# Optimization experiments

Hardware: AMD Instinct MI355X
Metric: run time of the kernel (lower is better)

## Reference

```python
import jax, jax.numpy as jnp
import numpy as np
import math


def setup_inputs() -> dict:
    key = jax.random.key(0)
    k1, k2 = jax.random.split(key)
    N, FEATS, K = 100000, 256, 2000
    node_embs = jax.random.normal(k1, (N, FEATS), dtype=jnp.float32)
    # mask of zeros = all nodes valid (original uses -inf for invalid nodes)
    mask = jnp.zeros((N, 1), dtype=jnp.float32)
    # scorer param, uniform(-stdv, stdv) with stdv = 1/sqrt(feats), as in reset_param
    stdv = 1.0 / math.sqrt(FEATS)
    scorer = jax.random.uniform(k2, (FEATS, 1), minval=-stdv, maxval=stdv, dtype=jnp.float32)
    return {"node_embs": node_embs, "mask": mask, "scorer": scorer, "k": K}


def reference(node_embs, mask, scorer, k):
    # scores: [N,1] = (node_embs @ scorer) / sum(scorer) + mask
    scores = (node_embs @ scorer) / jnp.sum(scorer) + mask
    # top-k over flattened scores (column dim is 1, so indices == node indices)
    vals, topk_indices = jax.lax.top_k(scores.ravel(), k)
    # NOTE: original filters vals > -inf (drops masked-out picks); with a finite
    # (all-zeros) mask every selected entry passes, so shape stays static [k].
    out = jnp.take(node_embs, topk_indices, axis=0)  # [k, feats]
    return out.T  # [feats, k]
```

## Files before the change

kernel.cpp:

```cpp
#include <hip/hip_runtime.h>
#include <stdint.h>


#define NBINS 8192
#define BIN_SHIFT 19
#define CAP 4096
#define HPARTS 8

__device__ __forceinline__ uint32_t f2key(float f) {
  uint32_t b = __float_as_uint(f);
  return (b & 0x80000000u) ? ~b : (b | 0x80000000u);
}

__global__ __launch_bounds__(256) void k1_scores(
    const float* __restrict__ embs, const float* __restrict__ mask,
    const float* __restrict__ scorer,
    uint32_t* __restrict__ keys, uint32_t* __restrict__ hdr, int N) {
  __shared__ float tile[32 * 132];
  __shared__ float sw[256];
  __shared__ float Ssh;
  int t = threadIdx.x;
  int r0 = blockIdx.x * 32;
  if (blockIdx.x == 0 && t < 16) hdr[t] = 0u;
  sw[t] = scorer[t];
  __syncthreads();
  if (t < 64) {
    double s = 0.0;
    for (int j = t; j < 256; j += 64) s += (double)sw[j];
#pragma unroll
    for (int off = 32; off >= 1; off >>= 1) s += __shfl_xor(s, off, 64);
    if (t == 0) Ssh = (float)s;
  }
  __syncthreads();
  float S = Ssh;
  int r = t >> 3, c = t & 7;
  float acc = 0.f;
  const float4* e4 = (const float4*)embs;
#pragma unroll
  for (int ch = 0; ch < 2; ++ch) {
    if (ch) __syncthreads();
#pragma unroll
    for (int m = 0; m < 4; ++m) {
      int flat = m * 256 + t;
      int rr = flat >> 5;
      int cc4 = flat & 31;
      int row = r0 + rr;
      float4 v = make_float4(0.f, 0.f, 0.f, 0.f);
      if (row < N) v = e4[(size_t)row * 64 + ch * 32 + cc4];
      float* dst = &tile[rr * 132 + cc4 * 4];
      dst[0] = v.x; dst[1] = v.y; dst[2] = v.z; dst[3] = v.w;
    }
    __syncthreads();
#pragma unroll
    for (int sl = 0; sl < 16; ++sl) {
      acc = fmaf(tile[r * 132 + c + 8 * sl], sw[ch * 128 + c + 8 * sl], acc);
    }
  }
  float m1 = acc + __shfl_xor(acc, 4, 64);
  float p1 = m1 + __shfl_xor(m1, 1, 64);
  float dot = p1 + __shfl_xor(p1, 2, 64);
  int row = r0 + r;
  if (c == 0 && row < N) {
    float score = dot / S + mask[row];
    keys[row] = f2key(score);
  }
}

__global__ __launch_bounds__(1024) void kHistFind(
    const uint32_t* __restrict__ keys, uint32_t* __restrict__ partials,
    uint32_t* __restrict__ hdr, int N, int k) {
  __shared__ uint32_t h[2][NBINS];
  __shared__ uint32_t wtot[16], wsuf[16];
  int t = threadIdx.x, bid = blockIdx.x;
  int lane = t & 63, wave = t >> 6;

  for (int i = t; i < 2 * NBINS; i += 1024) ((uint32_t*)h)[i] = 0u;
  __syncthreads();
  int per = (N + HPARTS - 1) / HPARTS;
  int lo = bid * per;
  int hi = lo + per; if (hi > N) hi = N;
  int sub = (t >> 7) & 1;
  int n4 = (hi - lo) >> 2;
  const uint4* q4 = (const uint4*)(keys + lo);
  for (int i = t; i < n4; i += 1024) {
    uint4 v = q4[i];
    atomicAdd(&h[sub][v.x >> BIN_SHIFT], 1u);
    atomicAdd(&h[sub][v.y >> BIN_SHIFT], 1u);
    atomicAdd(&h[sub][v.z >> BIN_SHIFT], 1u);
    atomicAdd(&h[sub][v.w >> BIN_SHIFT], 1u);
  }
  for (int i = lo + (n4 << 2) + t; i < hi; i += 1024)
    atomicAdd(&h[sub][keys[i] >> BIN_SHIFT], 1u);
  __syncthreads();
  uint32_t* dst = partials + (size_t)bid * NBINS;
  for (int i = t; i < NBINS; i += 1024) dst[i] = h[0][i] + h[1][i];
  __syncthreads();
  if (t == 0) {
    __threadfence();
    __hip_atomic_fetch_add(&hdr[8], 1u, __ATOMIC_ACQ_REL, __HIP_MEMORY_SCOPE_AGENT);
  }
  if (bid != 0) return;

  if (t == 0) {
    while (__hip_atomic_load(&hdr[8], __ATOMIC_ACQUIRE, __HIP_MEMORY_SCOPE_AGENT) < HPARTS)
      __builtin_amdgcn_s_sleep(8);
  }
  __syncthreads();

  uint32_t rb[8];
#pragma unroll
  for (int j = 0; j < 8; ++j) rb[j] = 0u;
#pragma unroll
  for (int pp = 0; pp < HPARTS; ++pp) {
    const uint4* q = (const uint4*)(partials + (size_t)pp * NBINS) + t * 2;
    uint4 a = q[0], b2 = q[1];
    rb[0] += a.x;  rb[1] += a.y;  rb[2] += a.z;  rb[3] += a.w;
    rb[4] += b2.x; rb[5] += b2.y; rb[6] += b2.z; rb[7] += b2.w;
  }
  uint32_t p8 = rb[0] + rb[1] + rb[2] + rb[3] + rb[4] + rb[5] + rb[6] + rb[7];
  uint32_t x = p8;
#pragma unroll
  for (int off = 1; off < 64; off <<= 1) {
    uint32_t v = __shfl_down(x, off, 64);
    if (lane + off < 64) x += v;
  }
  if (lane == 0) wtot[wave] = x;
  __syncthreads();
  if (t < 16) {
    uint32_t y = wtot[t];
#pragma unroll
    for (int off = 1; off < 16; off <<= 1) {
      uint32_t v = __shfl_down(y, off, 64);
      if (t + off < 16) y += v;
    }
    wsuf[t] = y - wtot[t];
  }
  __syncthreads();
  uint32_t St = x + wsuf[wave];
  uint32_t above = St - p8;
  if (above < (uint32_t)k && St >= (uint32_t)k) {
    uint32_t cum = above;
#pragma unroll
    for (int jj = 7; jj >= 0; --jj) {
      if (cum + rb[jj] >= (uint32_t)k) { hdr[0] = (uint32_t)(t * 8 + jj); hdr[1] = cum; break; }
      cum += rb[jj];
    }
  }
}

__global__ __launch_bounds__(256) void k3_compact(
    const uint32_t* __restrict__ keys, const uint32_t* __restrict__ hdr,
    uint32_t* __restrict__ ckey, uint32_t* __restrict__ cidx,
    uint32_t* __restrict__ counter, int N) {
  __shared__ uint32_t wcnt[4];
  __shared__ uint32_t wbase[4];
  __shared__ uint32_t blkbase;
  int i = blockIdx.x * 256 + threadIdx.x;
  int wave = threadIdx.x >> 6, lane = threadIdx.x & 63;
  uint32_t B = hdr[0];
  bool pred = false;
  uint32_t key = 0;
  if (i < N) {
    key = keys[i];
    pred = (key >> BIN_SHIFT) >= B;
  }
  unsigned long long ball = __ballot(pred);
  uint32_t prefix = (uint32_t)__popcll(ball & ((1ull << lane) - 1ull));
  if (lane == 0) wcnt[wave] = (uint32_t)__popcll(ball);
  __syncthreads();
  if (threadIdx.x == 0) {
    uint32_t tot = wcnt[0] + wcnt[1] + wcnt[2] + wcnt[3];
    blkbase = tot ? atomicAdd(counter, tot) : 0u;
    wbase[0] = 0;
    wbase[1] = wcnt[0];
    wbase[2] = wcnt[0] + wcnt[1];
    wbase[3] = wcnt[0] + wcnt[1] + wcnt[2];
  }
  __syncthreads();
  if (pred) {
    uint32_t pos = blkbase + wbase[wave] + prefix;
    if (pos < CAP) { ckey[pos] = key; cidx[pos] = (uint32_t)i; }
  }
}

__global__ __launch_bounds__(256) void k4_rank(
    const uint32_t* __restrict__ ckey, const uint32_t* __restrict__ cidx,
    const uint32_t* __restrict__ hdr, uint32_t* __restrict__ oidx, int k) {
  __shared__ uint32_t lk[CAP];
  __shared__ uint32_t li[CAP];
  uint32_t C = hdr[2];
  if (C > CAP) C = CAP;
  uint32_t base = blockIdx.x * 16u;
  if (base >= C) return;
  for (uint32_t j = threadIdx.x; j < C; j += 256u) {
    lk[j] = ckey[j];
    li[j] = cidx[j];
  }
  __syncthreads();
  int wave = threadIdx.x >> 6, lane = threadIdx.x & 63;
  uint32_t g0 = base + wave * 4u;
  uint32_t mk[4], mi[4], cnt[4];
#pragma unroll
  for (int q = 0; q < 4; ++q) {
    uint32_t g = g0 + q;
    bool valid = g < C;
    mk[q] = valid ? lk[g] : 0u;
    mi[q] = valid ? li[g] : 0xFFFFFFFFu;
    cnt[q] = 0u;
  }
  for (uint32_t j = lane; j < C; j += 64u) {
    uint32_t kj = lk[j], ij = li[j];
#pragma unroll
    for (int q = 0; q < 4; ++q)
      cnt[q] += (kj > mk[q] || (kj == mk[q] && ij < mi[q])) ? 1u : 0u;
  }
#pragma unroll
  for (int q = 0; q < 4; ++q) {
#pragma unroll
    for (int off = 32; off >= 1; off >>= 1) cnt[q] += __shfl_xor(cnt[q], off, 64);
  }
  if (lane == 0) {
#pragma unroll
    for (int q = 0; q < 4; ++q) {
      uint32_t g = g0 + q;
      if (g < C && cnt[q] < (uint32_t)k) oidx[cnt[q]] = mi[q];
    }
  }
}

__global__ __launch_bounds__(256) void k5_gather(
    const float* __restrict__ embs, const uint32_t* __restrict__ oidx,
    float* __restrict__ out, int k) {
  __shared__ float tile[16 * 132];
  __shared__ uint32_t sidx[16];
  int t = threadIdx.x;
  int r0 = blockIdx.x * 16;
  int fb = blockIdx.y * 128;
  if (t < 16) sidx[t] = (r0 + t < k) ? oidx[r0 + t] : 0u;
  __syncthreads();
  const float4* e4 = (const float4*)embs;
#pragma unroll
  for (int m = 0; m < 2; ++m) {
    int flat = m * 256 + t;
    int rr = flat >> 5;
    int cc4 = flat & 31;
    float4 v = e4[(size_t)sidx[rr] * 64 + (fb >> 2) + cc4];
    float* dst = &tile[rr * 132 + cc4 * 4];
    dst[0] = v.x; dst[1] = v.y; dst[2] = v.z; dst[3] = v.w;
  }
  __syncthreads();
  int fl = t >> 1;
  int rq = t & 1;
  float v[8];
#pragma unroll
  for (int i = 0; i < 8; ++i) v[i] = tile[(rq * 8 + i) * 132 + fl];
  size_t obase = (size_t)(fb + fl) * k + r0 + rq * 8;
  if (((k & 3) == 0) && (r0 + rq * 8 + 7 < k)) {
    *(float4*)(out + obase) = make_float4(v[0], v[1], v[2], v[3]);
    *(float4*)(out + obase + 4) = make_float4(v[4], v[5], v[6], v[7]);
  } else {
#pragma unroll
    for (int i = 0; i < 8; ++i)
      if (r0 + rq * 8 + i < k) out[obase + i] = v[i];
  }
}

extern "C" void kernel_launch(void* const* d_in, const int* in_sizes, int n_in,
                              void* d_out, int out_size, void* d_ws, size_t ws_size,
                              hipStream_t stream) {
  const float* embs = (const float*)d_in[0];
  const float* mask = (const float*)d_in[1];
  const float* scorer = (const float*)d_in[2];
  int F = in_sizes[2];
  int N = in_sizes[0] / F;
  int k = out_size / F;

  uint32_t* keys = (uint32_t*)d_out;
  uint32_t* partials = (uint32_t*)d_out + (out_size / 2);

  char* ws = (char*)d_ws;
  uint32_t* hdr = (uint32_t*)ws;
  uint32_t* ckey = (uint32_t*)(ws + 1024);
  uint32_t* cidx = ckey + CAP;
  uint32_t* oidx = cidx + CAP;

  k1_scores<<<(N + 31) / 32, 256, 0, stream>>>(embs, mask, scorer, keys, hdr, N);
  kHistFind<<<HPARTS, 1024, 0, stream>>>(keys, partials, hdr, N, k);
  k3_compact<<<(N + 255) / 256, 256, 0, stream>>>(keys, hdr, ckey, cidx, &hdr[2], N);
  k4_rank<<<(CAP + 15) / 16, 256, 0, stream>>>(ckey, cidx, hdr, oidx, k);
  k5_gather<<<dim3((k + 15) / 16, 2), 256, 0, stream>>>(embs, oidx, (float*)d_out, k);
}
```

Measured before the change: 48.10 us.

## Fuse histogram, threshold compaction and rank into one grid-synchronized kernel

Merges the histogram/threshold-find, compaction and rank-scatter kernels into a single 8-block persistent kernel. Blocks synchronize through global atomic counters and spin-waits instead of separate launches. The histogram shrinks to 4096 bins, which coarsens the threshold and can admit more candidates. The goal is to remove two kernel launches and their gaps. In exchange, compaction and the O(C^2) rank now run on only 8 blocks instead of hundreds, and correctness depends on all 8 blocks being co-resident.

```diff
diff --git a/kernel.cpp b/kernel.cpp
--- a/kernel.cpp
+++ b/kernel.cpp
@@ -2,8 +2,8 @@
 #include <stdint.h>
 
 
-#define NBINS 8192
-#define BIN_SHIFT 19
+#define NBINS 4096
+#define BIN_SHIFT 20
 #define CAP 4096
 #define HPARTS 8
 
@@ -66,11 +66,14 @@
   }
 }
 
-__global__ __launch_bounds__(1024) void kHistFind(
+__global__ __launch_bounds__(1024) void kSelAll(
     const uint32_t* __restrict__ keys, uint32_t* __restrict__ partials,
-    uint32_t* __restrict__ hdr, int N, int k) {
+    uint32_t* __restrict__ hdr, uint32_t* __restrict__ ckey,
+    uint32_t* __restrict__ cidx, uint32_t* __restrict__ oidx, int N, int k) {
   __shared__ uint32_t h[2][NBINS];
   __shared__ uint32_t wtot[16], wsuf[16];
+  __shared__ uint32_t wcnt[16], wbase[16];
+  __shared__ uint32_t blkbase;
   int t = threadIdx.x, bid = blockIdx.x;
   int lane = t & 63, wave = t >> 6;
 
@@ -99,131 +102,134 @@
     __threadfence();
     __hip_atomic_fetch_add(&hdr[8], 1u, __ATOMIC_ACQ_REL, __HIP_MEMORY_SCOPE_AGENT);
   }
-  if (bid != 0) return;
-
+
+  if (bid == 0) {
+    if (t == 0) {
+      while (__hip_atomic_load(&hdr[8], __ATOMIC_ACQUIRE, __HIP_MEMORY_SCOPE_AGENT) < HPARTS)
+        __builtin_amdgcn_s_sleep(8);
+    }
+    __syncthreads();
+    uint32_t rb[4];
+#pragma unroll
+    for (int j = 0; j < 4; ++j) rb[j] = 0u;
+#pragma unroll
+    for (int pp = 0; pp < HPARTS; ++pp) {
+      uint4 a = *((const uint4*)(partials + (size_t)pp * NBINS) + t);
+      rb[0] += a.x; rb[1] += a.y; rb[2] += a.z; rb[3] += a.w;
+    }
+    uint32_t p4 = rb[0] + rb[1] + rb[2] + rb[3];
+    uint32_t x = p4;
+#pragma unroll
+    for (int off = 1; off < 64; off <<= 1) {
+      uint32_t v = __shfl_down(x, off, 64);
+      if (lane + off < 64) x += v;
+    }
+    if (lane == 0) wtot[wave] = x;
+    __syncthreads();
+    if (t < 16) {
+      uint32_t y = wtot[t];
+#pragma unroll
+      for (int off = 1; off < 16; off <<= 1) {
+        uint32_t v = __shfl_down(y, off, 64);
+        if (t + off < 16) y += v;
+      }
+      wsuf[t] = y - wtot[t];
+    }
+    __syncthreads();
+    uint32_t St = x + wsuf[wave];
+    uint32_t above = St - p4;
+    if (above < (uint32_t)k && St >= (uint32_t)k) {
+      uint32_t cum = above;
+#pragma unroll
+      for (int jj = 3; jj >= 0; --jj) {
+        if (cum + rb[jj] >= (uint32_t)k) {
+          hdr[0] = (uint32_t)(t * 4 + jj);
+          hdr[1] = cum;
+          __threadfence();
+          __hip_atomic_fetch_add(&hdr[9], 1u, __ATOMIC_ACQ_REL, __HIP_MEMORY_SCOPE_AGENT);
+          break;
+        }
+        cum += rb[jj];
+      }
+    }
+    __syncthreads();
+  } else {
+    if (t == 0) {
+      while (__hip_atomic_load(&hdr[9], __ATOMIC_ACQUIRE, __HIP_MEMORY_SCOPE_AGENT) < 1u)
+        __builtin_amdgcn_s_sleep(8);
+    }
+    __syncthreads();
+  }
+  uint32_t B = hdr[0];
+
+  int niter = (per + 1023) >> 10;
+  for (int it = 0; it < niter; ++it) {
+    int i = lo + (it << 10) + t;
+    bool pred = false;
+    uint32_t key = 0;
+    if (i < hi) {
+      key = keys[i];
+      pred = (key >> BIN_SHIFT) >= B;
+    }
+    unsigned long long ball = __ballot(pred);
+    uint32_t prefix = (uint32_t)__popcll(ball & ((1ull << lane) - 1ull));
+    if (lane == 0) wcnt[wave] = (uint32_t)__popcll(ball);
+    __syncthreads();
+    if (t == 0) {
+      uint32_t tot = 0;
+#pragma unroll
+      for (int w = 0; w < 16; ++w) { wbase[w] = tot; tot += wcnt[w]; }
+      blkbase = tot ? atomicAdd(&hdr[2], tot) : 0u;
+    }
+    __syncthreads();
+    if (pred) {
+      uint32_t pos = blkbase + wbase[wave] + prefix;
+      if (pos < CAP) { ckey[pos] = key; cidx[pos] = (uint32_t)i; }
+    }
+    __syncthreads();
+  }
   if (t == 0) {
-    while (__hip_atomic_load(&hdr[8], __ATOMIC_ACQUIRE, __HIP_MEMORY_SCOPE_AGENT) < HPARTS)
+    __threadfence();
+    __hip_atomic_fetch_add(&hdr[10], 1u, __ATOMIC_ACQ_REL, __HIP_MEMORY_SCOPE_AGENT);
+    while (__hip_atomic_load(&hdr[10], __ATOMIC_ACQUIRE, __HIP_MEMORY_SCOPE_AGENT) < HPARTS)
       __builtin_amdgcn_s_sleep(8);
   }
   __syncthreads();
 
-  uint32_t rb[8];
-#pragma unroll
-  for (int j = 0; j < 8; ++j) rb[j] = 0u;
-#pragma unroll
-  for (int pp = 0; pp < HPARTS; ++pp) {
-    const uint4* q = (const uint4*)(partials + (size_t)pp * NBINS) + t * 2;
-    uint4 a = q[0], b2 = q[1];
-    rb[0] += a.x;  rb[1] += a.y;  rb[2] += a.z;  rb[3] += a.w;
-    rb[4] += b2.x; rb[5] += b2.y; rb[6] += b2.z; rb[7] += b2.w;
-  }
-  uint32_t p8 = rb[0] + rb[1] + rb[2] + rb[3] + rb[4] + rb[5] + rb[6] + rb[7];
-  uint32_t x = p8;
-#pragma unroll
-  for (int off = 1; off < 64; off <<= 1) {
-    uint32_t v = __shfl_down(x, off, 64);
-    if (lane + off < 64) x += v;
-  }
-  if (lane == 0) wtot[wave] = x;
-  __syncthreads();
-  if (t < 16) {
-    uint32_t y = wtot[t];
-#pragma unroll
-    for (int off = 1; off < 16; off <<= 1) {
-      uint32_t v = __shfl_down(y, off, 64);
-      if (t + off < 16) y += v;
-    }
-    wsuf[t] = y - wtot[t];
-  }
-  __syncthreads();
-  uint32_t St = x + wsuf[wave];
-  uint32_t above = St - p8;
-  if (above < (uint32_t)k && St >= (uint32_t)k) {
-    uint32_t cum = above;
-#pragma unroll
-    for (int jj = 7; jj >= 0; --jj) {
-      if (cum + rb[jj] >= (uint32_t)k) { hdr[0] = (uint32_t)(t * 8 + jj); hdr[1] = cum; break; }
-      cum += rb[jj];
-    }
-  }
-}
-
-__global__ __launch_bounds__(256) void k3_compact(
-    const uint32_t* __restrict__ keys, const uint32_t* __restrict__ hdr,
-    uint32_t* __restrict__ ckey, uint32_t* __restrict__ cidx,
-    uint32_t* __restrict__ counter, int N) {
-  __shared__ uint32_t wcnt[4];
-  __shared__ uint32_t wbase[4];
-  __shared__ uint32_t blkbase;
-  int i = blockIdx.x * 256 + threadIdx.x;
-  int wave = threadIdx.x >> 6, lane = threadIdx.x & 63;
-  uint32_t B = hdr[0];
-  bool pred = false;
-  uint32_t key = 0;
-  if (i < N) {
-    key = keys[i];
-    pred = (key >> BIN_SHIFT) >= B;
-  }
-  unsigned long long ball = __ballot(pred);
-  uint32_t prefix = (uint32_t)__popcll(ball & ((1ull << lane) - 1ull));
-  if (lane == 0) wcnt[wave] = (uint32_t)__popcll(ball);
-  __syncthreads();
-  if (threadIdx.x == 0) {
-    uint32_t tot = wcnt[0] + wcnt[1] + wcnt[2] + wcnt[3];
-    blkbase = tot ? atomicAdd(counter, tot) : 0u;
-    wbase[0] = 0;
-    wbase[1] = wcnt[0];
-    wbase[2] = wcnt[0] + wcnt[1];
-    wbase[3] = wcnt[0] + wcnt[1] + wcnt[2];
-  }
-  __syncthreads();
-  if (pred) {
-    uint32_t pos = blkbase + wbase[wave] + prefix;
-    if (pos < CAP) { ckey[pos] = key; cidx[pos] = (uint32_t)i; }
-  }
-}
-
-__global__ __launch_bounds__(256) void k4_rank(
-    const uint32_t* __restrict__ ckey, const uint32_t* __restrict__ cidx,
-    const uint32_t* __restrict__ hdr, uint32_t* __restrict__ oidx, int k) {
-  __shared__ uint32_t lk[CAP];
-  __shared__ uint32_t li[CAP];
   uint32_t C = hdr[2];
   if (C > CAP) C = CAP;
-  uint32_t base = blockIdx.x * 16u;
-  if (base >= C) return;
-  for (uint32_t j = threadIdx.x; j < C; j += 256u) {
-    lk[j] = ckey[j];
-    li[j] = cidx[j];
-  }
-  __syncthreads();
-  int wave = threadIdx.x >> 6, lane = threadIdx.x & 63;
-  uint32_t g0 = base + wave * 4u;
-  uint32_t mk[4], mi[4], cnt[4];
-#pragma unroll
-  for (int q = 0; q < 4; ++q) {
-    uint32_t g = g0 + q;
-    bool valid = g < C;
-    mk[q] = valid ? lk[g] : 0u;
-    mi[q] = valid ? li[g] : 0xFFFFFFFFu;
-    cnt[q] = 0u;
-  }
-  for (uint32_t j = lane; j < C; j += 64u) {
-    uint32_t kj = lk[j], ij = li[j];
-#pragma unroll
-    for (int q = 0; q < 4; ++q)
-      cnt[q] += (kj > mk[q] || (kj == mk[q] && ij < mi[q])) ? 1u : 0u;
-  }
-#pragma unroll
-  for (int q = 0; q < 4; ++q) {
-#pragma unroll
-    for (int off = 32; off >= 1; off >>= 1) cnt[q] += __shfl_xor(cnt[q], off, 64);
-  }
-  if (lane == 0) {
+  uint32_t* lk = &h[0][0];
+  uint32_t* li = &h[1][0];
+  for (uint32_t j = t; j < C; j += 1024u) { lk[j] = ckey[j]; li[j] = cidx[j]; }
+  __syncthreads();
+  uint32_t wid = (uint32_t)bid * 16u + (uint32_t)wave;
+  for (uint32_t g0 = wid * 4u; g0 < C; g0 += 128u * 4u) {
+    uint32_t mk[4], mi[4], cnt[4];
 #pragma unroll
     for (int q = 0; q < 4; ++q) {
       uint32_t g = g0 + q;
-      if (g < C && cnt[q] < (uint32_t)k) oidx[cnt[q]] = mi[q];
+      bool valid = g < C;
+      mk[q] = valid ? lk[g] : 0u;
+      mi[q] = valid ? li[g] : 0xFFFFFFFFu;
+      cnt[q] = 0u;
+    }
+    for (uint32_t j = lane; j < C; j += 64u) {
+      uint32_t kj = lk[j], ij = li[j];
+#pragma unroll
+      for (int q = 0; q < 4; ++q)
+        cnt[q] += (kj > mk[q] || (kj == mk[q] && ij < mi[q])) ? 1u : 0u;
+    }
+#pragma unroll
+    for (int q = 0; q < 4; ++q) {
+#pragma unroll
+      for (int off = 32; off >= 1; off >>= 1) cnt[q] += __shfl_xor(cnt[q], off, 64);
+    }
+    if (lane == 0) {
+#pragma unroll
+      for (int q = 0; q < 4; ++q) {
+        uint32_t g = g0 + q;
+        if (g < C && cnt[q] < (uint32_t)k) oidx[cnt[q]] = mi[q];
+      }
     }
   }
 }
@@ -285,8 +291,6 @@
   uint32_t* oidx = cidx + CAP;
 
   k1_scores<<<(N + 31) / 32, 256, 0, stream>>>(embs, mask, scorer, keys, hdr, N);
-  kHistFind<<<HPARTS, 1024, 0, stream>>>(keys, partials, hdr, N, k);
-  k3_compact<<<(N + 255) / 256, 256, 0, stream>>>(keys, hdr, ckey, cidx, &hdr[2], N);
-  k4_rank<<<(CAP + 15) / 16, 256, 0, stream>>>(ckey, cidx, hdr, oidx, k);
+  kSelAll<<<HPARTS, 1024, 0, stream>>>(keys, partials, hdr, ckey, cidx, oidx, N, k);
   k5_gather<<<dim3((k + 15) / 16, 2), 256, 0, stream>>>(embs, oidx, (float*)d_out, k);
 }
```

Result: slower. 79.81 us (+65.9%).
